# Optimization experiments

Hardware: AMD Instinct MI355X
Metric: run time of the kernel (lower is better)

The kernel has to match this reference:

```python
import jax, jax.numpy as jnp
import numpy as np

EMB = 768
HID = 3072
HID2 = 2 * HID
NE = 8
K = 2
B, N = 8, 2048


def setup_inputs() -> dict:
    key = jax.random.key(0)
    ks = jax.random.split(key, 9)
    s = lambda *d: 1.0 / np.sqrt(d[-2])  # ~ torch Linear init scale
    inp = {
        'x': jax.random.normal(ks[0], (B, N, EMB), dtype=jnp.float32),
        'Wg': jax.random.normal(ks[1], (EMB, NE), dtype=jnp.float32) * (1.0 / np.sqrt(EMB)),
        'bg': jnp.zeros((NE,), dtype=jnp.float32),
        'W1': jax.random.normal(ks[2], (NE, EMB, HID), dtype=jnp.float32) * (1.0 / np.sqrt(EMB)),
        'b1': jnp.zeros((NE, HID), dtype=jnp.float32),
        'W2': jax.random.normal(ks[3], (NE, HID, HID2), dtype=jnp.float32) * (1.0 / np.sqrt(HID)),
        'b2': jnp.zeros((NE, HID2), dtype=jnp.float32),
        'W3': jax.random.normal(ks[4], (NE, HID2, EMB), dtype=jnp.float32) * (1.0 / np.sqrt(HID2)),
        'b3': jnp.zeros((NE, EMB), dtype=jnp.float32),
    }
    return inp


def _gelu(x):
    return jax.nn.gelu(x, approximate=False)  # torch nn.GELU default (erf)


def reference(x, Wg, bg, W1, b1, W2, b2, W3, b3):
    # gating: top-k over expert scores, softmax over the k selected logits
    scores = x @ Wg + bg                     # [B,N,NE]
    topk_vals, topk_idx = jax.lax.top_k(scores, K)   # [B,N,K]
    gates = jax.nn.softmax(topk_vals, axis=-1)       # [B,N,K]
    # dense combine weights: c[b,n,e] = sum_i gates[...,i] * (idx[...,i]==e)
    onehot = jax.nn.one_hot(topk_idx, NE, dtype=x.dtype)  # [B,N,K,NE]
    comb = jnp.einsum('bnk,bnke->bne', gates, onehot)     # [B,N,NE]
    out = jnp.zeros_like(x)
    for e in range(NE):  # small fixed expert loop
        h = _gelu(x @ W1[e] + b1[e])       # [B,N,HID]
        h = _gelu(h @ W2[e] + b2[e])       # [B,N,HID2]
        y = h @ W3[e] + b3[e]              # [B,N,EMB]
        out = out + comb[..., e:e + 1] * y
    return out
```

## Files before the change

kernel.cpp:

```cpp
#include <hip/hip_runtime.h>
#include <hip/hip_bf16.h>

#define EMB 768
#define HID 3072
#define HID2 6144
#define NE 8
#define TOK 16384
#define SLOTS 32768
#define SLACK 256
#define MAXTILES 136

typedef __attribute__((ext_vector_type(8))) short bf16x8;
typedef __attribute__((ext_vector_type(4))) float f32x4;

__device__ __forceinline__ unsigned short bfbits(float f) {
  __hip_bfloat16 h = __float2bfloat16(f);
  return __builtin_bit_cast(unsigned short, h);
}


__global__ void k_init(int* counts, int* fill) {
  if (threadIdx.x < NE) { counts[threadIdx.x] = 0; fill[threadIdx.x] = 0; }
}

__global__ __launch_bounds__(256) void k_gating(
    const float* __restrict__ x, const float* __restrict__ Wg,
    const float* __restrict__ bg, int* __restrict__ eidx,
    float* __restrict__ gates)
{
  const int wave = threadIdx.x >> 6, lane = threadIdx.x & 63;
  const int t = blockIdx.x * 4 + wave;
  const float* xr = x + (size_t)t * EMB;
  float p[NE];
#pragma unroll
  for (int e = 0; e < NE; ++e) p[e] = 0.f;
  for (int k = lane; k < EMB; k += 64) {
    const float xv = xr[k];
    const float* wr = Wg + (size_t)k * NE;
#pragma unroll
    for (int e = 0; e < NE; ++e) p[e] += xv * wr[e];
  }
#pragma unroll
  for (int e = 0; e < NE; ++e) {
#pragma unroll
    for (int o = 32; o > 0; o >>= 1) p[e] += __shfl_xor(p[e], o);
    p[e] += bg[e];
  }
  float v0 = -1e30f, v1 = -1e30f; int i0 = 0, i1 = 0;
#pragma unroll
  for (int e = 0; e < NE; ++e) {
    const float v = p[e];
    if (v > v0)      { v1 = v0; i1 = i0; v0 = v; i0 = e; }
    else if (v > v1) { v1 = v;  i1 = e; }
  }
  const float ex = expf(v1 - v0);
  const float g0 = 1.f / (1.f + ex);
  const float g1 = 1.f - g0;
  if (lane == 0) {
    eidx[2*t] = i0; eidx[2*t+1] = i1;
    gates[2*t] = g0; gates[2*t+1] = g1;
  }
}

__global__ __launch_bounds__(256) void k_count(const int* __restrict__ eidx,
                                               int* __restrict__ counts)
{
  __shared__ int bins[NE];
  if (threadIdx.x < NE) bins[threadIdx.x] = 0;
  __syncthreads();
  const int base = blockIdx.x * 512 + threadIdx.x * 2;
  atomicAdd(&bins[eidx[base]], 1);
  atomicAdd(&bins[eidx[base + 1]], 1);
  __syncthreads();
  if (threadIdx.x < NE) atomicAdd(&counts[threadIdx.x], bins[threadIdx.x]);
}

__global__ void k_offsets(const int* __restrict__ counts, int* __restrict__ offsets,
                          int* __restrict__ tmap)
{
  offsets[0] = 0;
  int idx = 0;
  for (int e = 0; e < NE; ++e) {
    offsets[e+1] = offsets[e] + counts[e];
    const int nt = (counts[e] + 255) >> 8;
    for (int i = 0; i < nt; ++i) tmap[idx++] = (e << 16) | i;
  }
  for (; idx < MAXTILES; ++idx) tmap[idx] = -1;
}

__global__ __launch_bounds__(256) void k_route(
    const int* __restrict__ eidx, int* __restrict__ fill,
    const int* __restrict__ offsets, int* __restrict__ route_tok,
    float* __restrict__ gate_slot, int* __restrict__ tok_k,
    const float* __restrict__ gates)
{
  __shared__ int bins[NE], base[NE];
  const int tid = threadIdx.x;
  if (tid < NE) bins[tid] = 0;
  __syncthreads();
  const int t = blockIdx.x * 256 + tid;
  int e0 = eidx[2*t], e1 = eidx[2*t+1];
  int lp0 = atomicAdd(&bins[e0], 1);
  int lp1 = atomicAdd(&bins[e1], 1);
  __syncthreads();
  if (tid < NE) base[tid] = atomicAdd(&fill[tid], bins[tid]);
  __syncthreads();
  const int s0 = offsets[e0] + base[e0] + lp0;
  const int s1 = offsets[e1] + base[e1] + lp1;
  route_tok[s0] = t;          route_tok[s1] = t;
  gate_slot[s0] = gates[2*t]; gate_slot[s1] = gates[2*t+1];
  tok_k[s0] = 2*t;            tok_k[s1] = 2*t + 1;
}

__global__ __launch_bounds__(256) void k_gather(
    const float* __restrict__ x, const int* __restrict__ route_tok,
    __hip_bfloat16* __restrict__ xg)
{
  const int w = threadIdx.x >> 6, lane = threadIdx.x & 63;
  const int s = blockIdx.x * 4 + w;
  const int t = route_tok[s];
  const float4* src = (const float4*)(x + (size_t)t * EMB);
  unsigned short* dst = (unsigned short*)xg + (size_t)s * EMB;
#pragma unroll
  for (int i = 0; i < 3; ++i) {
    const float4 v = src[lane + 64 * i];
    ushort4 u;
    u.x = bfbits(v.x); u.y = bfbits(v.y); u.z = bfbits(v.z); u.w = bfbits(v.w);
    *(ushort4*)(dst + (lane + 64 * i) * 4) = u;
  }
}

#define NT1 (NE * (HID  / 64) * (EMB  / 64))
#define NT2 (NE * (HID2 / 64) * (HID  / 64))
#define NT3 (NE * (EMB  / 64) * (HID2 / 64))

typedef __attribute__((ext_vector_type(8))) unsigned short u16x8;

__global__ __launch_bounds__(256) void k_transpose_all(
    const float* __restrict__ W1, const float* __restrict__ W2,
    const float* __restrict__ W3, __hip_bfloat16* __restrict__ Wb1,
    __hip_bfloat16* __restrict__ Wb2, __hip_bfloat16* __restrict__ Wb3)
{
  __shared__ float tile[64][65];
  int bid = blockIdx.x;
  const float* W; __hip_bfloat16* Wt; int K, N;
  if (bid < NT1)              { W = W1; Wt = Wb1; K = EMB;  N = HID;  }
  else if (bid < NT1 + NT2)   { W = W2; Wt = Wb2; K = HID;  N = HID2; bid -= NT1; }
  else                        { W = W3; Wt = Wb3; K = HID2; N = EMB;  bid -= NT1 + NT2; }
  const int ntn = N >> 6, ntk = K >> 6;
  const int e  = bid / (ntn * ntk);
  const int rem = bid - e * (ntn * ntk);
  const int k0 = (rem / ntn) << 6;
  const int n0 = (rem % ntn) << 6;

  const float* Wp = W + (size_t)e * K * N;
  __hip_bfloat16* Wtp = Wt + (size_t)e * K * N;
  const int tx = threadIdx.x, ty = threadIdx.y;

  const int q = tx & 15, rsub = tx >> 4;
#pragma unroll
  for (int it = 0; it < 4; ++it) {
    const int r = it * 16 + ty * 2 + rsub;
    const float4 v = *(const float4*)(Wp + (size_t)(k0 + r) * N + n0 + 4 * q);
    tile[r][4 * q]     = v.x;
    tile[r][4 * q + 1] = v.y;
    tile[r][4 * q + 2] = v.z;
    tile[r][4 * q + 3] = v.w;
  }
  __syncthreads();
  const int q8 = tx & 7, r8 = tx >> 3;
#pragma unroll
  for (int it = 0; it < 2; ++it) {
    const int n = it * 32 + ty * 4 + r8;
    u16x8 u;
#pragma unroll
    for (int j = 0; j < 8; ++j) u[j] = bfbits(tile[8 * q8 + j][n]);
    *(u16x8*)((unsigned short*)Wtp + (size_t)(n0 + n) * K + k0 + 8 * q8) = u;
  }
}


#define BARRIER() asm volatile("s_barrier" ::: "memory")
#define LGKM(n) { asm volatile("s_waitcnt lgkmcnt(" #n ")" ::: "memory"); __builtin_amdgcn_sched_barrier(0); }
#define VMC(n)  { asm volatile("s_waitcnt vmcnt(" #n ")" ::: "memory"); __builtin_amdgcn_sched_barrier(0); }

template<bool GELU, bool OUTBF, bool SCATTER>
__global__ __launch_bounds__(512) void ffn_gemm8(
    const __hip_bfloat16* __restrict__ A,
    const __hip_bfloat16* __restrict__ Bt,
    const float* __restrict__ bias,
    void* __restrict__ Cout,
    const int* __restrict__ counts,
    const int* __restrict__ offsets,
    const int* __restrict__ tmap,
    const float* __restrict__ gate_slot,
    const int* __restrict__ tok_k,
    int K, int N)
{
  const int me = tmap[blockIdx.y];
  if (me < 0) return;
  const int e  = me >> 16;
  const int m0 = (me & 0xffff) << 8;
  const int cnt = counts[e];
  const int seg = offsets[e];
  const int n0 = blockIdx.x * 256;

  __shared__ char lds[131072];

  const int tid = threadIdx.x;
  const int wave = tid >> 6, lane = tid & 63;
  const int wm = wave >> 2, wn = wave & 3;

  const size_t KB = (size_t)K * 2;
  const char* Ag = (const char*)(A + (size_t)(seg + m0) * K);
  const char* Bg = (const char*)(Bt + (size_t)e * N * K + (size_t)n0 * K);

  const int s_r  = tid >> 2;
  const int s_cb = ((tid & 3) * 16) ^ (((s_r >> 1) & 3) << 4);

  auto S = [&](int x) {
    const int ub = (x & 3) * 32768;
    const int kbyte = x * 64;
    const char* sa = Ag + (size_t)s_r * KB + kbyte + s_cb;
    const char* sb = Bg + (size_t)s_r * KB + kbyte + s_cb;
    __builtin_amdgcn_global_load_lds(
        (const __attribute__((address_space(1))) void*)sa,
        (__attribute__((address_space(3))) void*)(lds + ub + tid * 16), 16, 0, 0);
    __builtin_amdgcn_global_load_lds(
        (const __attribute__((address_space(1))) void*)(sa + 128 * KB),
        (__attribute__((address_space(3))) void*)(lds + ub + 8192 + tid * 16), 16, 0, 0);
    __builtin_amdgcn_global_load_lds(
        (const __attribute__((address_space(1))) void*)sb,
        (__attribute__((address_space(3))) void*)(lds + ub + 16384 + tid * 16), 16, 0, 0);
    __builtin_amdgcn_global_load_lds(
        (const __attribute__((address_space(1))) void*)(sb + 128 * KB),
        (__attribute__((address_space(3))) void*)(lds + ub + 16384 + 8192 + tid * 16), 16, 0, 0);
  };

  const int fr    = lane & 15;
  const int coff  = ((lane >> 4) * 16) ^ (((fr >> 1) & 3) << 4);
  const int aoff0 = (wm * 128 + fr) * 64 + coff;
  const int boff0 = 16384 + (wn * 64 + fr) * 64 + coff;

  f32x4 acc[8][4];
#pragma unroll
  for (int i = 0; i < 8; ++i)
#pragma unroll
    for (int j = 0; j < 4; ++j)
      acc[i][j] = (f32x4){0.f, 0.f, 0.f, 0.f};

  const int NPH = K >> 5;

  bf16x8 aE[8], bE[4], aO[8], bO[4];

#define RD(x, as, bs) {                                             \
    const char* ub_ = lds + ((x) & 3) * 32768;                      \
    _Pragma("unroll")                                               \
    for (int m_ = 0; m_ < 8; ++m_)                                  \
      as[m_] = *(const bf16x8*)(ub_ + aoff0 + m_ * 1024);           \
    _Pragma("unroll")                                               \
    for (int n_ = 0; n_ < 4; ++n_)                                  \
      bs[n_] = *(const bf16x8*)(ub_ + boff0 + n_ * 1024); }

#define MM(as, bs) {                                                \
    _Pragma("unroll")                                               \
    for (int m_ = 0; m_ < 8; ++m_)                                  \
      _Pragma("unroll")                                             \
      for (int n_ = 0; n_ < 4; ++n_)                                \
        acc[m_][n_] = __builtin_amdgcn_mfma_f32_16x16x32_bf16(      \
            as[m_], bs[n_], acc[m_][n_], 0, 0, 0); }

  S(0); S(1);
  VMC(4);
  BARRIER();

  RD(0, aE, bE);
  S(2);
  VMC(4);
  BARRIER();

  RD(1, aO, bO);
  S(3);
  LGKM(12);
  MM(aE, bE);
  VMC(4);
  BARRIER();

  for (int p = 2; p < NPH; p += 2) {
    RD(p, aE, bE);
    S(p + 2 < NPH ? p + 2 : NPH - 1);
    LGKM(12);
    MM(aO, bO);
    VMC(4);
    BARRIER();
    RD(p + 1, aO, bO);
    S(p + 3 < NPH ? p + 3 : NPH - 1);
    LGKM(12);
    MM(aE, bE);
    VMC(4);
    BARRIER();
  }

  LGKM(0);
  MM(aO, bO);

#undef RD
#undef MM

#pragma unroll
  for (int mf = 0; mf < 8; ++mf) {
#pragma unroll
    for (int r2 = 0; r2 < 4; ++r2) {
      const int gm = m0 + wm * 128 + mf * 16 + (lane >> 4) * 4 + r2;
      if (gm >= cnt) continue;
      if (SCATTER) {
        const int s = seg + gm;
        const float g = gate_slot[s];
        const int tk = tok_k[s];
        float* dst = (float*)Cout + ((size_t)(tk & 1) * TOK + (size_t)(tk >> 1)) * EMB;
#pragma unroll
        for (int nf = 0; nf < 4; ++nf) {
          const int gcol = n0 + wn * 64 + nf * 16 + fr;
          dst[gcol] = g * (acc[mf][nf][r2] + bias[(size_t)e * N + gcol]);
        }
      } else {
#pragma unroll
        for (int nf = 0; nf < 4; ++nf) {
          const int gcol = n0 + wn * 64 + nf * 16 + fr;
          float v = acc[mf][nf][r2] + bias[(size_t)e * N + gcol];
          if (GELU) v = 0.5f * v * (1.0f + erff(v * 0.70710678118654752f));
          if (OUTBF)
            ((__hip_bfloat16*)Cout)[(size_t)(seg + gm) * N + gcol] = __float2bfloat16(v);
          else
            ((float*)Cout)[(size_t)(seg + gm) * N + gcol] = v;
        }
      }
    }
  }
}

__global__ __launch_bounds__(256) void k_combine2(const float* __restrict__ ybuf2,
                                                  float* __restrict__ out)
{
  const size_t total = (size_t)TOK * EMB / 4;
  for (size_t i = blockIdx.x * 256 + threadIdx.x; i < total; i += (size_t)gridDim.x * 256) {
    const float4 a = ((const float4*)ybuf2)[i];
    const float4 b = ((const float4*)(ybuf2 + (size_t)TOK * EMB))[i];
    float4 o;
    o.x = a.x + b.x; o.y = a.y + b.y; o.z = a.z + b.z; o.w = a.w + b.w;
    ((float4*)out)[i] = o;
  }
}


extern "C" void kernel_launch(void* const* d_in, const int* in_sizes, int n_in,
                              void* d_out, int out_size, void* d_ws, size_t ws_size,
                              hipStream_t stream)
{
  const float* x  = (const float*)d_in[0];
  const float* Wg = (const float*)d_in[1];
  const float* bg = (const float*)d_in[2];
  const float* W1 = (const float*)d_in[3];
  const float* b1 = (const float*)d_in[4];
  const float* W2 = (const float*)d_in[5];
  const float* b2 = (const float*)d_in[6];
  const float* W3 = (const float*)d_in[7];
  const float* b3 = (const float*)d_in[8];
  float* out = (float*)d_out;

  char* ws = (char*)d_ws;
  size_t off = 0;
  auto alloc = [&](size_t bytes) -> void* {
    void* p = ws + off;
    off = (off + bytes + 255) & ~(size_t)255;
    return p;
  };

  int*   counts    = (int*)alloc(NE * 4);
  int*   fill      = (int*)alloc(NE * 4);
  int*   offsets   = (int*)alloc((NE + 1) * 4);
  int*   tmap      = (int*)alloc(MAXTILES * 4);
  int*   eidx      = (int*)alloc((size_t)TOK * 2 * 4);
  float* gates     = (float*)alloc((size_t)TOK * 2 * 4);
  int*   route_tok = (int*)alloc((size_t)SLOTS * 4);
  float* gate_slot = (float*)alloc((size_t)(SLOTS + SLACK) * 4);
  int*   tok_k     = (int*)alloc((size_t)(SLOTS + SLACK) * 4);
  __hip_bfloat16* Wb1 = (__hip_bfloat16*)alloc((size_t)NE * EMB  * HID  * 2);
  __hip_bfloat16* Wb2 = (__hip_bfloat16*)alloc((size_t)NE * HID  * HID2 * 2);
  __hip_bfloat16* Wb3 = (__hip_bfloat16*)alloc((size_t)NE * HID2 * EMB  * 2);
  __hip_bfloat16* xg  = (__hip_bfloat16*)alloc((size_t)(SLOTS + SLACK) * EMB  * 2);
  __hip_bfloat16* h1  = (__hip_bfloat16*)alloc((size_t)(SLOTS + SLACK) * HID  * 2);
  __hip_bfloat16* h2  = (__hip_bfloat16*)alloc((size_t)(SLOTS + SLACK) * HID2 * 2);
  float*          ybuf2 = (float*)alloc((size_t)2 * TOK * EMB * 4);
  (void)ws_size; (void)in_sizes; (void)n_in; (void)out_size;

  k_init<<<1, 64, 0, stream>>>(counts, fill);
  k_gating<<<TOK / 4, 256, 0, stream>>>(x, Wg, bg, eidx, gates);
  k_count<<<SLOTS / 512, 256, 0, stream>>>(eidx, counts);
  k_offsets<<<1, 1, 0, stream>>>(counts, offsets, tmap);
  k_route<<<TOK / 256, 256, 0, stream>>>(eidx, fill, offsets, route_tok,
                                         gate_slot, tok_k, gates);
  k_gather<<<SLOTS / 4, 256, 0, stream>>>(x, route_tok, xg);

  k_transpose_all<<<NT1 + NT2 + NT3, dim3(32, 8), 0, stream>>>(W1, W2, W3, Wb1, Wb2, Wb3);

  ffn_gemm8<true,  true,  false><<<dim3(HID  / 256, MAXTILES), 512, 0, stream>>>(
      xg, Wb1, b1, h1, counts, offsets, tmap, nullptr, nullptr, EMB,  HID);
  ffn_gemm8<true,  true,  false><<<dim3(HID2 / 256, MAXTILES), 512, 0, stream>>>(
      h1, Wb2, b2, h2, counts, offsets, tmap, nullptr, nullptr, HID,  HID2);
  ffn_gemm8<false, false, true ><<<dim3(EMB  / 256, MAXTILES), 512, 0, stream>>>(
      h2, Wb3, b3, ybuf2, counts, offsets, tmap, gate_slot, tok_k, HID2, EMB);

  k_combine2<<<2048, 256, 0, stream>>>(ybuf2, out);
}
```

Measured before the change: 2.434 ms.

## Split-K the third expert GEMM and accumulate into output with atomics

The final down-projection GEMM (K=6144, N=768) had only 3 column tiles per row tile, so it launched few blocks. It now splits K four ways via a z grid dimension, and each split atomically adds its gated partial result straight into the zeroed output, with the bias added only by split zero. This removes the two-slot scratch buffer and the separate combine kernel. The cost is a memset of the output and many fp32 atomic adds, and the order of floating-point accumulation is no longer deterministic.

After: 2.746 ms. +12.8%, slower.

```diff
diff --git a/kernel.cpp b/kernel.cpp
--- a/kernel.cpp
+++ b/kernel.cpp
@@ -184,7 +184,7 @@
 #define LGKM(n) { asm volatile("s_waitcnt lgkmcnt(" #n ")" ::: "memory"); __builtin_amdgcn_sched_barrier(0); }
 #define VMC(n)  { asm volatile("s_waitcnt vmcnt(" #n ")" ::: "memory"); __builtin_amdgcn_sched_barrier(0); }
 
-template<bool GELU, bool OUTBF, bool SCATTER>
+template<bool GELU, bool OUTBF, bool ATOMIC>
 __global__ __launch_bounds__(512) void ffn_gemm8(
     const __hip_bfloat16* __restrict__ A,
     const __hip_bfloat16* __restrict__ Bt,
@@ -195,7 +195,7 @@
     const int* __restrict__ tmap,
     const float* __restrict__ gate_slot,
     const int* __restrict__ tok_k,
-    int K, int N)
+    int K, int N, int KLEN)
 {
   const int me = tmap[blockIdx.y];
   if (me < 0) return;
@@ -204,6 +204,7 @@
   const int cnt = counts[e];
   const int seg = offsets[e];
   const int n0 = blockIdx.x * 256;
+  const int kbase = blockIdx.z * KLEN * 2;
 
   __shared__ char lds[131072];
 
@@ -220,7 +221,7 @@
 
   auto S = [&](int x) {
     const int ub = (x & 3) * 32768;
-    const int kbyte = x * 64;
+    const int kbyte = kbase + x * 64;
     const char* sa = Ag + (size_t)s_r * KB + kbyte + s_cb;
     const char* sb = Bg + (size_t)s_r * KB + kbyte + s_cb;
     __builtin_amdgcn_global_load_lds(
@@ -249,7 +250,7 @@
     for (int j = 0; j < 4; ++j)
       acc[i][j] = (f32x4){0.f, 0.f, 0.f, 0.f};
 
-  const int NPH = K >> 5;
+  const int NPH = KLEN >> 5;
 
   bf16x8 aE[8], bE[4], aO[8], bO[4];
 
@@ -313,15 +314,17 @@
     for (int r2 = 0; r2 < 4; ++r2) {
       const int gm = m0 + wm * 128 + mf * 16 + (lane >> 4) * 4 + r2;
       if (gm >= cnt) continue;
-      if (SCATTER) {
+      if (ATOMIC) {
         const int s = seg + gm;
         const float g = gate_slot[s];
-        const int tk = tok_k[s];
-        float* dst = (float*)Cout + ((size_t)(tk & 1) * TOK + (size_t)(tk >> 1)) * EMB;
+        const int tok = tok_k[s] >> 1;
+        float* dst = (float*)Cout + (size_t)tok * EMB;
+        const bool addb = (blockIdx.z == 0);
 #pragma unroll
         for (int nf = 0; nf < 4; ++nf) {
           const int gcol = n0 + wn * 64 + nf * 16 + fr;
-          dst[gcol] = g * (acc[mf][nf][r2] + bias[(size_t)e * N + gcol]);
+          const float v = acc[mf][nf][r2] + (addb ? bias[(size_t)e * N + gcol] : 0.f);
+          atomicAdd(&dst[gcol], g * v);
         }
       } else {
 #pragma unroll
@@ -336,19 +339,6 @@
         }
       }
     }
-  }
-}
-
-__global__ __launch_bounds__(256) void k_combine2(const float* __restrict__ ybuf2,
-                                                  float* __restrict__ out)
-{
-  const size_t total = (size_t)TOK * EMB / 4;
-  for (size_t i = blockIdx.x * 256 + threadIdx.x; i < total; i += (size_t)gridDim.x * 256) {
-    const float4 a = ((const float4*)ybuf2)[i];
-    const float4 b = ((const float4*)(ybuf2 + (size_t)TOK * EMB))[i];
-    float4 o;
-    o.x = a.x + b.x; o.y = a.y + b.y; o.z = a.z + b.z; o.w = a.w + b.w;
-    ((float4*)out)[i] = o;
   }
 }
 
@@ -391,8 +381,9 @@
   __hip_bfloat16* xg  = (__hip_bfloat16*)alloc((size_t)(SLOTS + SLACK) * EMB  * 2);
   __hip_bfloat16* h1  = (__hip_bfloat16*)alloc((size_t)(SLOTS + SLACK) * HID  * 2);
   __hip_bfloat16* h2  = (__hip_bfloat16*)alloc((size_t)(SLOTS + SLACK) * HID2 * 2);
-  float*          ybuf2 = (float*)alloc((size_t)2 * TOK * EMB * 4);
-  (void)ws_size; (void)in_sizes; (void)n_in; (void)out_size;
+  (void)ws_size; (void)in_sizes; (void)n_in;
+
+  hipMemsetAsync(d_out, 0, (size_t)out_size * 4, stream);
 
   k_init<<<1, 64, 0, stream>>>(counts, fill);
   k_gating<<<TOK / 4, 256, 0, stream>>>(x, Wg, bg, eidx, gates);
@@ -405,11 +396,9 @@
   k_transpose_all<<<NT1 + NT2 + NT3, dim3(32, 8), 0, stream>>>(W1, W2, W3, Wb1, Wb2, Wb3);
 
   ffn_gemm8<true,  true,  false><<<dim3(HID  / 256, MAXTILES), 512, 0, stream>>>(
-      xg, Wb1, b1, h1, counts, offsets, tmap, nullptr, nullptr, EMB,  HID);
+      xg, Wb1, b1, h1, counts, offsets, tmap, nullptr, nullptr, EMB,  HID,  EMB);
   ffn_gemm8<true,  true,  false><<<dim3(HID2 / 256, MAXTILES), 512, 0, stream>>>(
-      h1, Wb2, b2, h2, counts, offsets, tmap, nullptr, nullptr, HID,  HID2);
-  ffn_gemm8<false, false, true ><<<dim3(EMB  / 256, MAXTILES), 512, 0, stream>>>(
-      h2, Wb3, b3, ybuf2, counts, offsets, tmap, gate_slot, tok_k, HID2, EMB);
-
-  k_combine2<<<2048, 256, 0, stream>>>(ybuf2, out);
-}
+      h1, Wb2, b2, h2, counts, offsets, tmap, nullptr, nullptr, HID,  HID2, HID);
+  ffn_gemm8<false, false, true ><<<dim3(EMB  / 256, MAXTILES, 4), 512, 0, stream>>>(
+      h2, Wb3, b3, out, counts, offsets, tmap, gate_slot, tok_k, HID2, EMB, HID2 / 4);
+}
```
